# Kernel optimization log

Hardware: AMD Instinct MI355X
Metric: run time of the kernel (lower is better)

## Reference

```python
import jax, jax.numpy as jnp
import numpy as np

B = 524288
H = 20          # heads
NUM_EX = 13     # embedding rows
EMB = 3         # embedding dim
FEAT_IN, FEAT_OUT = 3, 5
HEAD_IN, HEAD_HID = 8, 10


def setup_inputs() -> dict:
    key = jax.random.key(0)
    ks = jax.random.split(key, 12)
    e = jax.random.randint(ks[0], (B, H), 0, NUM_EX)
    f = jax.random.normal(ks[1], (B, H * FEAT_IN), dtype=jnp.float32)
    # embedding table; row 0 zeroed as in the torch __init__
    emb = jax.random.normal(ks[2], (NUM_EX, EMB), dtype=jnp.float32) * 0.1
    emb = emb.at[0].set(0.0)
    # features Linear(3 -> 5), stored as (in, out) so y = x @ Wf + bf
    Wf = jax.random.normal(ks[3], (FEAT_IN, FEAT_OUT), dtype=jnp.float32) * 0.5
    bf = jax.random.normal(ks[4], (FEAT_OUT,), dtype=jnp.float32) * 0.1
    # 20 parallel head MLPs, batched over the head axis
    W1 = jax.random.normal(ks[5], (H, HEAD_IN, HEAD_HID), dtype=jnp.float32) * 0.3
    b1 = jax.random.normal(ks[6], (H, HEAD_HID), dtype=jnp.float32) * 0.1
    W2 = jax.random.normal(ks[7], (H, HEAD_HID), dtype=jnp.float32) * 0.3
    b2 = jax.random.normal(ks[8], (H,), dtype=jnp.float32) * 0.1
    # output Linear(20 -> 1)
    Wo = jax.random.normal(ks[9], (H, 1), dtype=jnp.float32) * 0.3
    bo = jax.random.normal(ks[10], (1,), dtype=jnp.float32) * 0.1
    return {"e": e, "f": f, "emb": emb, "Wf": Wf, "bf": bf,
            "W1": W1, "b1": b1, "W2": W2, "b2": b2, "Wo": Wo, "bo": bo}


def reference(e, f, emb, Wf, bf, W1, b1, W2, b2, Wo, bo):
    ev = emb[e]                                    # (B, 20, 3) embedding lookup
    fv = f.reshape(-1, H, FEAT_IN) @ Wf + bf       # (B, 20, 5)
    x = jnp.concatenate([ev, fv], axis=2)          # (B, 20, 8)
    # all 20 heads as one batched matmul instead of a Python loop
    h1 = jax.nn.leaky_relu(jnp.einsum('bhi,hio->bho', x, W1) + b1)  # (B, 20, 10)
    h = jax.nn.softplus(jnp.einsum('bho,ho->bh', h1, W2) + b2)      # (B, 20)
    return h @ Wo + bo                             # (B, 1)
```

## Files before the change

### kernel.cpp

```cpp
#include <hip/hip_runtime.h>


#define HH   20
#define NEX  13
#define TST  12
#define WS_M 0
#define WS_T 640
#define NT   512

typedef __attribute__((ext_vector_type(4))) _Float16 half4;

__device__ __forceinline__ float softplus_fast(float x) {
    return fmaxf(x, 0.0f) + __logf(1.0f + __expf(-fabsf(x)));
}

__global__ void airfit_setup(const float* __restrict__ emb,
                             const float* __restrict__ Wf,
                             const float* __restrict__ bf,
                             const float* __restrict__ W1,
                             const float* __restrict__ b1,
                             float* __restrict__ ws)
{
    int t = blockIdx.x * 256 + threadIdx.x;
    if (t < HH * 3 * 10) {
        int h = t / 30, c = (t / 10) % 3, o = t % 10;
        float a = 0.0f;
        for (int q = 0; q < 5; ++q)
            a += Wf[c * 5 + q] * W1[(h * 8 + 3 + q) * 10 + o];
        ws[WS_M + (h * 3 + c) * 10 + o] = a;
    }
    if (t < HH * NEX * 10) {
        int h = t / (NEX * 10), idx = (t / 10) % NEX, o = t % 10;
        float a = b1[h * 10 + o];
        for (int i = 0; i < 3; ++i)
            a += emb[idx * 3 + i] * W1[(h * 8 + i) * 10 + o];
        for (int q = 0; q < 5; ++q)
            a += bf[q] * W1[(h * 8 + 3 + q) * 10 + o];
        ws[WS_T + (h * NEX + idx) * TST + o] = a;
    }
}

__global__ __launch_bounds__(NT, 4) void airfit_kernel(
    const int*   __restrict__ e,   const float* __restrict__ f,
    const float* __restrict__ ws,  const float* __restrict__ W2,
    const float* __restrict__ b2,  const float* __restrict__ Wo,
    const float* __restrict__ bo,  float* __restrict__ out, int B)
{
    __shared__ half4          s_fh[15][NT];
    __shared__ unsigned short s_e[NT * 6];
    __shared__ float          s_T[HH * NEX * TST];

    const int tid  = threadIdx.x;
    const int base = blockIdx.x * NT;
    const int nIt  = min(NT, B - base);

    for (int t = tid; t < HH * NEX * TST; t += NT)
        s_T[t] = ws[WS_T + t];

    {
        const float4* fg = reinterpret_cast<const float4*>(f) + (size_t)base * 15;
        const int total4 = nIt * 15;
#pragma unroll
        for (int k = 0; k < 15; ++k) {
            int idx = tid + NT * k;
            if (idx < total4) {
                float4 v = fg[idx];
                int item = idx / 15, c4 = idx - item * 15;
                half4 hv = { (_Float16)v.x, (_Float16)v.y,
                             (_Float16)v.z, (_Float16)v.w };
                s_fh[c4][item] = hv;
            }
        }
    }

    {
        const int4* eg = reinterpret_cast<const int4*>(e) + (size_t)base * 5;
        const int total4 = nIt * 5;
#pragma unroll
        for (int k = 0; k < 5; ++k) {
            int idx = tid + NT * k;
            if (idx < total4) {
                int4 iv = eg[idx];
                int item = idx / 5, g = idx - item * 5;
                unsigned p = (unsigned)iv.x | ((unsigned)iv.y << 4) |
                             ((unsigned)iv.z << 8) | ((unsigned)iv.w << 12);
                s_e[item * 6 + g] = (unsigned short)p;
            }
        }
    }

    __syncthreads();

    if (tid >= nIt) return;
    const float* M = ws + WS_M;

    const unsigned* e32 = reinterpret_cast<const unsigned*>(s_e);
    unsigned ew[3] = { e32[tid * 3 + 0], e32[tid * 3 + 1], e32[tid * 3 + 2] };

    float acc = bo[0];

#pragma unroll
    for (int g = 0; g < 5; ++g) {
        half4 a0 = s_fh[3 * g + 0][tid];
        half4 a1 = s_fh[3 * g + 1][tid];
        half4 a2 = s_fh[3 * g + 2][tid];
        float ff[12] = { (float)a0.x, (float)a0.y, (float)a0.z, (float)a0.w,
                         (float)a1.x, (float)a1.y, (float)a1.z, (float)a1.w,
                         (float)a2.x, (float)a2.y, (float)a2.z, (float)a2.w };
        unsigned gw  = ew[g >> 1] >> ((g & 1) * 16);

#pragma unroll
        for (int t = 0; t < 4; ++t) {
            const int h = 4 * g + t;
            int idx = (gw >> (4 * t)) & 0xf;

            const float* Trow = s_T + (h * NEX + idx) * TST;
            float4 t0 = *reinterpret_cast<const float4*>(Trow);
            float4 t1 = *reinterpret_cast<const float4*>(Trow + 4);
            float2 t2 = *reinterpret_cast<const float2*>(Trow + 8);
            float pre[10] = { t0.x, t0.y, t0.z, t0.w,
                              t1.x, t1.y, t1.z, t1.w, t2.x, t2.y };

            float g0 = ff[3 * t + 0], g1 = ff[3 * t + 1], g2 = ff[3 * t + 2];
            float hacc = b2[h];
#pragma unroll
            for (int o = 0; o < 10; ++o) {
                float a = pre[o];
                a = fmaf(g0, M[(h * 3 + 0) * 10 + o], a);
                a = fmaf(g1, M[(h * 3 + 1) * 10 + o], a);
                a = fmaf(g2, M[(h * 3 + 2) * 10 + o], a);
                a = fmaxf(a, 0.01f * a);
                hacc = fmaf(a, W2[h * 10 + o], hacc);
            }
            acc = fmaf(softplus_fast(hacc), Wo[h], acc);
        }
    }

    out[base + tid] = acc;
}

extern "C" void kernel_launch(void* const* d_in, const int* in_sizes, int n_in,
                              void* d_out, int out_size, void* d_ws, size_t ws_size,
                              hipStream_t stream) {
    const int*   e   = (const int*)  d_in[0];
    const float* f   = (const float*)d_in[1];
    const float* emb = (const float*)d_in[2];
    const float* Wf  = (const float*)d_in[3];
    const float* bf  = (const float*)d_in[4];
    const float* W1  = (const float*)d_in[5];
    const float* b1  = (const float*)d_in[6];
    const float* W2  = (const float*)d_in[7];
    const float* b2  = (const float*)d_in[8];
    const float* Wo  = (const float*)d_in[9];
    const float* bo  = (const float*)d_in[10];
    float* out = (float*)d_out;
    float* ws  = (float*)d_ws;

    int B = in_sizes[0] / HH;

    airfit_setup<<<11, 256, 0, stream>>>(emb, Wf, bf, W1, b1, ws);

    int blocks = (B + NT - 1) / NT;
    airfit_kernel<<<blocks, NT, 0, stream>>>(e, f, ws, W2, b2, Wo, bo, out, B);
}
```

Measured before the change: 253.4 us.

## Split heads across two blocks per chunk and combine outputs with atomics

Each batch chunk is now handled by two blocks, each covering 10 of the 20 heads. This halves shared memory per block and raises the launch-bound occupancy target so more blocks fit per CU. Partial sums are combined with atomicAdd into an output that the setup kernel pre-fills with the output bias, which makes the setup kernel sweep the whole output. Block-index remapping places paired half-blocks near each other, and the embedding-table stride is padded to 13. Costs added: atomic traffic, an extra full-output write pass, narrower float2/int2 global loads, and per-element table reads from LDS instead of vector loads.

```diff
diff --git a/kernel.cpp b/kernel.cpp
--- a/kernel.cpp
+++ b/kernel.cpp
@@ -3,12 +3,13 @@
 
 #define HH   20
 #define NEX  13
-#define TST  12
+#define TST  13
+#define HHF  10
 #define WS_M 0
 #define WS_T 640
 #define NT   512
 
-typedef __attribute__((ext_vector_type(4))) _Float16 half4;
+typedef __attribute__((ext_vector_type(2))) _Float16 half2v;
 
 __device__ __forceinline__ float softplus_fast(float x) {
     return fmaxf(x, 0.0f) + __logf(1.0f + __expf(-fabsf(x)));
@@ -19,7 +20,9 @@
                              const float* __restrict__ bf,
                              const float* __restrict__ W1,
                              const float* __restrict__ b1,
-                             float* __restrict__ ws)
+                             const float* __restrict__ bo,
+                             float* __restrict__ ws,
+                             float* __restrict__ out, int B)
 {
     int t = blockIdx.x * 256 + threadIdx.x;
     if (t < HH * 3 * 10) {
@@ -29,62 +32,87 @@
             a += Wf[c * 5 + q] * W1[(h * 8 + 3 + q) * 10 + o];
         ws[WS_M + (h * 3 + c) * 10 + o] = a;
     }
-    if (t < HH * NEX * 10) {
-        int h = t / (NEX * 10), idx = (t / 10) % NEX, o = t % 10;
-        float a = b1[h * 10 + o];
-        for (int i = 0; i < 3; ++i)
-            a += emb[idx * 3 + i] * W1[(h * 8 + i) * 10 + o];
-        for (int q = 0; q < 5; ++q)
-            a += bf[q] * W1[(h * 8 + 3 + q) * 10 + o];
-        ws[WS_T + (h * NEX + idx) * TST + o] = a;
+    if (t < HH * NEX * TST) {
+        int h = t / (NEX * TST);
+        int r = t - h * (NEX * TST);
+        int idx = r / TST, o = r - idx * TST;
+        float a = 0.0f;
+        if (o < 10) {
+            a = b1[h * 10 + o];
+            for (int i = 0; i < 3; ++i)
+                a += emb[idx * 3 + i] * W1[(h * 8 + i) * 10 + o];
+            for (int q = 0; q < 5; ++q)
+                a += bf[q] * W1[(h * 8 + 3 + q) * 10 + o];
+        }
+        ws[WS_T + t] = a;
+    }
+    int nv4 = B >> 2;
+    float bov = bo[0];
+    if (t < nv4) {
+        float4 v = { bov, bov, bov, bov };
+        reinterpret_cast<float4*>(out)[t] = v;
+    } else if (t == nv4) {
+        for (int i = nv4 * 4; i < B; ++i) out[i] = bov;
     }
 }
 
-__global__ __launch_bounds__(NT, 4) void airfit_kernel(
+__global__ __launch_bounds__(NT, 8) void airfit_kernel(
     const int*   __restrict__ e,   const float* __restrict__ f,
     const float* __restrict__ ws,  const float* __restrict__ W2,
     const float* __restrict__ b2,  const float* __restrict__ Wo,
-    const float* __restrict__ bo,  float* __restrict__ out, int B)
+    float* __restrict__ out, int B)
 {
-    __shared__ half4          s_fh[15][NT];
-    __shared__ unsigned short s_e[NT * 6];
-    __shared__ float          s_T[HH * NEX * TST];
+    __shared__ half2v        s_f[5][NT][3];
+    __shared__ unsigned int  s_e32[NT];
+    __shared__ unsigned char s_e8[NT];
+    __shared__ float         s_T[HHF * NEX * TST];
 
-    const int tid  = threadIdx.x;
-    const int base = blockIdx.x * NT;
+    const int tid = threadIdx.x;
+    const int bid = blockIdx.x, nB = gridDim.x;
+    int chunk, hf;
+    if ((nB & 15) == 0) {
+        chunk = ((bid >> 4) << 3) | (bid & 7);
+        hf    = (bid >> 3) & 1;
+    } else {
+        chunk = bid >> 1;
+        hf    = bid & 1;
+    }
+    const int base = chunk * NT;
     const int nIt  = min(NT, B - base);
 
-    for (int t = tid; t < HH * NEX * TST; t += NT)
-        s_T[t] = ws[WS_T + t];
+    for (int t = tid; t < HHF * NEX * TST; t += NT)
+        s_T[t] = ws[WS_T + hf * (HHF * NEX * TST) + t];
 
     {
-        const float4* fg = reinterpret_cast<const float4*>(f) + (size_t)base * 15;
-        const int total4 = nIt * 15;
+        const float2* fg = reinterpret_cast<const float2*>(f);
+        const int fbase  = base * 30 + hf * 15;
+        const int total2 = nIt * 15;
 #pragma unroll
         for (int k = 0; k < 15; ++k) {
             int idx = tid + NT * k;
-            if (idx < total4) {
-                float4 v = fg[idx];
-                int item = idx / 15, c4 = idx - item * 15;
-                half4 hv = { (_Float16)v.x, (_Float16)v.y,
-                             (_Float16)v.z, (_Float16)v.w };
-                s_fh[c4][item] = hv;
+            if (idx < total2) {
+                int item = idx / 15, c2 = idx - item * 15;
+                float2 v = fg[fbase + item * 30 + c2];
+                int g = c2 / 3, j = c2 - 3 * g;
+                s_f[g][item][j] = half2v{ (_Float16)v.x, (_Float16)v.y };
             }
         }
     }
 
     {
-        const int4* eg = reinterpret_cast<const int4*>(e) + (size_t)base * 5;
-        const int total4 = nIt * 5;
+        const int2* eg = reinterpret_cast<const int2*>(e);
+        const int ebase  = base * 10 + hf * 5;
+        const int total2 = nIt * 5;
 #pragma unroll
         for (int k = 0; k < 5; ++k) {
             int idx = tid + NT * k;
-            if (idx < total4) {
-                int4 iv = eg[idx];
-                int item = idx / 5, g = idx - item * 5;
-                unsigned p = (unsigned)iv.x | ((unsigned)iv.y << 4) |
-                             ((unsigned)iv.z << 8) | ((unsigned)iv.w << 12);
-                s_e[item * 6 + g] = (unsigned short)p;
+            if (idx < total2) {
+                int item = idx / 5, p = idx - item * 5;
+                int2 v = eg[ebase + item * 10 + p];
+                unsigned char pk =
+                    (unsigned char)((v.x & 0xf) | ((v.y & 0xf) << 4));
+                if (p < 4) ((unsigned char*)s_e32)[item * 4 + p] = pk;
+                else       s_e8[item] = pk;
             }
         }
     }
@@ -92,40 +120,35 @@
     __syncthreads();
 
     if (tid >= nIt) return;
-    const float* M = ws + WS_M;
 
-    const unsigned* e32 = reinterpret_cast<const unsigned*>(s_e);
-    unsigned ew[3] = { e32[tid * 3 + 0], e32[tid * 3 + 1], e32[tid * 3 + 2] };
+    const float* M  = ws + WS_M;
+    const int    hb = hf * HHF;
 
-    float acc = bo[0];
+    unsigned ed = s_e32[tid];
+    unsigned eb = s_e8[tid];
+
+    float acc = 0.0f;
+#pragma unroll
+    for (int g = 0; g < 5; ++g) {
+        half2v a0 = s_f[g][tid][0];
+        half2v a1 = s_f[g][tid][1];
+        half2v a2 = s_f[g][tid][2];
+        float ff[6] = { (float)a0.x, (float)a0.y, (float)a1.x,
+                        (float)a1.y, (float)a2.x, (float)a2.y };
 
 #pragma unroll
-    for (int g = 0; g < 5; ++g) {
-        half4 a0 = s_fh[3 * g + 0][tid];
-        half4 a1 = s_fh[3 * g + 1][tid];
-        half4 a2 = s_fh[3 * g + 2][tid];
-        float ff[12] = { (float)a0.x, (float)a0.y, (float)a0.z, (float)a0.w,
-                         (float)a1.x, (float)a1.y, (float)a1.z, (float)a1.w,
-                         (float)a2.x, (float)a2.y, (float)a2.z, (float)a2.w };
-        unsigned gw  = ew[g >> 1] >> ((g & 1) * 16);
-
-#pragma unroll
-        for (int t = 0; t < 4; ++t) {
-            const int h = 4 * g + t;
-            int idx = (gw >> (4 * t)) & 0xf;
-
-            const float* Trow = s_T + (h * NEX + idx) * TST;
-            float4 t0 = *reinterpret_cast<const float4*>(Trow);
-            float4 t1 = *reinterpret_cast<const float4*>(Trow + 4);
-            float2 t2 = *reinterpret_cast<const float2*>(Trow + 8);
-            float pre[10] = { t0.x, t0.y, t0.z, t0.w,
-                              t1.x, t1.y, t1.z, t1.w, t2.x, t2.y };
+        for (int t = 0; t < 2; ++t) {
+            const int hl = 2 * g + t;
+            const int h  = hb + hl;
+            unsigned idx = (hl < 8) ? ((ed >> (4 * hl)) & 0xfu)
+                                    : ((eb >> (4 * (hl - 8))) & 0xfu);
+            const float* Trow = s_T + (hl * NEX + idx) * TST;
 
             float g0 = ff[3 * t + 0], g1 = ff[3 * t + 1], g2 = ff[3 * t + 2];
             float hacc = b2[h];
 #pragma unroll
             for (int o = 0; o < 10; ++o) {
-                float a = pre[o];
+                float a = Trow[o];
                 a = fmaf(g0, M[(h * 3 + 0) * 10 + o], a);
                 a = fmaf(g1, M[(h * 3 + 1) * 10 + o], a);
                 a = fmaf(g2, M[(h * 3 + 2) * 10 + o], a);
@@ -136,7 +159,7 @@
         }
     }
 
-    out[base + tid] = acc;
+    atomicAdd(out + base + tid, acc);
 }
 
 extern "C" void kernel_launch(void* const* d_in, const int* in_sizes, int n_in,
@@ -158,8 +181,11 @@
 
     int B = in_sizes[0] / HH;
 
-    airfit_setup<<<11, 256, 0, stream>>>(emb, Wf, bf, W1, b1, ws);
+    int sblocks = ((B >> 2) + 1 + 255) / 256;
+    int minb    = (HH * NEX * TST + 255) / 256;
+    if (sblocks < minb) sblocks = minb;
+    airfit_setup<<<sblocks, 256, 0, stream>>>(emb, Wf, bf, W1, b1, bo, ws, out, B);
 
-    int blocks = (B + NT - 1) / NT;
-    airfit_kernel<<<blocks, NT, 0, stream>>>(e, f, ws, W2, b2, Wo, bo, out, B);
+    int nChunks = (B + NT - 1) / NT;
+    airfit_kernel<<<2 * nChunks, NT, 0, stream>>>(e, f, ws, W2, b2, Wo, out, B);
 }
```

New measurement: 247.0 us. 2.5% less time.
